# Kernel optimization log

Hardware: AMD Instinct MI355X
Metric: run time of the kernel (lower is better)

## Reference

```python
import jax, jax.numpy as jnp
import numpy as np

N_HEAD = 16
P_MIN, P_MAX = 1e-4, 1e3
V_MIN = 1e-10
SHIFT = 5.0


def setup_inputs() -> dict:
    key = jax.random.key(0)
    ks = jax.random.split(key, 4)
    B, T, C = 2, 2048, 1024
    x = jax.random.normal(ks[0], (B, T, C), dtype=jnp.float32)
    w_attn = jax.random.normal(ks[1], (C, 3 * C), dtype=jnp.float32) * 0.02
    b_attn = jnp.zeros((3 * C,), dtype=jnp.float32)
    w_proj = jax.random.normal(ks[2], (C, C), dtype=jnp.float32) * 0.02
    b_proj = jnp.zeros((C,), dtype=jnp.float32)
    p_param = jnp.ones((C,), dtype=jnp.float32)
    return {"x": x, "w_attn": w_attn, "b_attn": b_attn,
            "w_proj": w_proj, "b_proj": b_proj, "p_param": p_param}


def reference(x, w_attn, b_attn, w_proj, b_proj, p_param):
    B, T, C = x.shape
    H = N_HEAD
    d = C // H

    qkv = x @ w_attn + b_attn                      # [B,T,3C]
    q, k, v = jnp.split(qkv, 3, axis=2)

    # signed, clamped power exponent per channel: (sign(p)+0.5).sign() * clamp(|p|)
    p = jnp.sign(jnp.sign(p_param) + 0.5) * jnp.clip(jnp.abs(p_param), P_MIN, P_MAX)

    # log-power transform of V with max-subtraction over T for stability
    v = jnp.clip(jnp.abs(v + SHIFT), V_MIN, None)  # [B,T,C]
    z = p * jnp.log(v)
    z_max = jnp.max(z, axis=1, keepdims=True)      # [B,1,C]
    v = jnp.exp(z - z_max)

    # heads: [B,H,T,d]
    q = q.reshape(B, T, H, d).transpose(0, 2, 1, 3)
    k = k.reshape(B, T, H, d).transpose(0, 2, 1, 3)
    v = v.reshape(B, T, H, d).transpose(0, 2, 1, 3)

    scale = 1.0 / jnp.sqrt(jnp.float32(d))
    scores = jnp.einsum('bhqd,bhkd->bhqk', q, k) * scale
    causal = jnp.tril(jnp.ones((T, T), dtype=bool))
    scores = jnp.where(causal, scores, -jnp.inf)
    att = jax.nn.softmax(scores, axis=-1)
    mean = jnp.einsum('bhqk,bhkd->bhqd', att, v)   # [B,H,T,d]
    mean = mean.transpose(0, 2, 1, 3).reshape(B, T, C)

    # invert the log-power transform (generalized power mean)
    y = jnp.exp((z_max + jnp.log(mean)) / p) - SHIFT
    return y @ w_proj + b_proj
```

## Files before the change

### kernel.cpp

```cpp
#include <hip/hip_runtime.h>
#include <hip/hip_bf16.h>
#include <math.h>

constexpr int B_ = 2;
constexpr int T_ = 2048;
constexpr int C_ = 1024;
constexpr int H_ = 16;
constexpr int D_ = 64;
constexpr int M_ = B_ * T_;
constexpr float SHIFT_ = 5.0f;
constexpr float P_MIN_ = 1e-4f;
constexpr float P_MAX_ = 1e3f;
constexpr float V_MIN_ = 1e-10f;
typedef __attribute__((ext_vector_type(8))) short s16x8;
typedef __attribute__((ext_vector_type(4))) short s16x4;
typedef __attribute__((ext_vector_type(8))) _Float16 h16x8;
typedef __attribute__((ext_vector_type(4))) float f32x4;
typedef unsigned short ushort_t;

__device__ __forceinline__ float clamp_p(float pp) {
    float s = (pp >= 0.f) ? 1.f : -1.f;
    return s * fminf(fmaxf(fabsf(pp), P_MIN_), P_MAX_);
}

__device__ __forceinline__ ushort_t f2h(float f) {
    _Float16 h = (_Float16)f;
    return __builtin_bit_cast(unsigned short, h);
}
__device__ __forceinline__ float h2f(ushort_t h) {
    return (float)__builtin_bit_cast(_Float16, h);
}

__device__ __forceinline__ float fast_exp2(float x) {
#if __has_builtin(__builtin_amdgcn_exp2f)
    return __builtin_amdgcn_exp2f(x);
#else
    return __expf(x * 0.6931471805599453f);
#endif
}

__device__ __forceinline__ void gload_lds16(const void* g, void* l) {
    __builtin_amdgcn_global_load_lds(
        (const __attribute__((address_space(1))) unsigned int*)g,
        (__attribute__((address_space(3))) unsigned int*)l, 16, 0, 0);
}

__global__ __launch_bounds__(256)
void conv_h(const float* __restrict__ src, ushort_t* __restrict__ hi) {
    int idx = blockIdx.x * 256 + threadIdx.x;
    float4 f = ((const float4*)src)[idx];
    ushort4 h;
    h.x = f2h(f.x); h.y = f2h(f.y); h.z = f2h(f.z); h.w = f2h(f.w);
    ((ushort4*)hi)[idx] = h;
}

__global__ __launch_bounds__(256)
void convT_h(const float* __restrict__ W, ushort_t* __restrict__ Wth,
             int N, int K) {
    __shared__ float tile[64][65];
    const int k0 = blockIdx.y * 64, n0 = blockIdx.x * 64;
    const int tr = threadIdx.x >> 4;
    const int tc4 = (threadIdx.x & 15) * 4;
#pragma unroll
    for (int i = 0; i < 4; ++i) {
        float4 f = *(const float4*)&W[(size_t)(k0 + tr + i * 16) * N + n0 + tc4];
        tile[tr + i * 16][tc4 + 0] = f.x;
        tile[tr + i * 16][tc4 + 1] = f.y;
        tile[tr + i * 16][tc4 + 2] = f.z;
        tile[tr + i * 16][tc4 + 3] = f.w;
    }
    __syncthreads();
#pragma unroll
    for (int i = 0; i < 4; ++i) {
        int n = tr + i * 16;
        ushort4 h;
        h.x = f2h(tile[tc4 + 0][n]);
        h.y = f2h(tile[tc4 + 1][n]);
        h.z = f2h(tile[tc4 + 2][n]);
        h.w = f2h(tile[tc4 + 3][n]);
        *(ushort4*)&Wth[(size_t)(n0 + n) * K + k0 + tc4] = h;
    }
}

__global__ __launch_bounds__(256)
void gemm1(const ushort_t* __restrict__ Ah, const ushort_t* __restrict__ Bh,
           const float* __restrict__ bias, float* __restrict__ Cm,
           int M, int N, int K) {
    __shared__ ushort_t Lds[2 * 2 * 128 * 32];

    const int tid = threadIdx.x;
    const int w = tid >> 6;
    const int lane = tid & 63;
    const int l16 = lane & 15;
    const int quad = lane >> 4;
    const int row0 = blockIdx.y * 128, col0 = blockIdx.x * 128;
    const int wr = w >> 1, wc = w & 1;

    const ushort_t* gb[8];
    ushort_t* lb[8];
#pragma unroll
    for (int j = 0; j < 8; ++j) {
        int q = j * 4 + w;
        int plane = q >> 4;
        int cc = q & 15;
        int sub = cc & 1;
        int r = (cc >> 1) * 16 + (lane >> 2);
        const ushort_t* src = plane ? Bh : Ah;
        int tb = plane ? col0 : row0;
        gb[j] = src + (size_t)(tb + r) * K + sub * 32 + (lane & 3) * 8;
        lb[j] = &Lds[plane * 8192 + sub * 4096 + r * 32 + (lane & 3) * 8];
    }

    f32x4 acc[4][4] = {};

    for (int k0 = 0; k0 < K; k0 += 64) {
        __syncthreads();
#pragma unroll
        for (int j = 0; j < 8; ++j)
            gload_lds16(gb[j] + k0, lb[j]);
        __syncthreads();

#pragma unroll
        for (int kk = 0; kk < 2; ++kk) {
            h16x8 af[4], bf[4];
#pragma unroll
            for (int mi = 0; mi < 4; ++mi)
                af[mi] = *(const h16x8*)&Lds[kk * 4096 + (wr * 64 + mi * 16 + l16) * 32 + quad * 8];
#pragma unroll
            for (int ni = 0; ni < 4; ++ni)
                bf[ni] = *(const h16x8*)&Lds[8192 + kk * 4096 + (wc * 64 + ni * 16 + l16) * 32 + quad * 8];
#pragma unroll
            for (int mi = 0; mi < 4; ++mi)
#pragma unroll
                for (int ni = 0; ni < 4; ++ni)
                    acc[mi][ni] = __builtin_amdgcn_mfma_f32_16x16x32_f16(af[mi], bf[ni], acc[mi][ni], 0, 0, 0);
        }
    }

#pragma unroll
    for (int mi = 0; mi < 4; ++mi) {
#pragma unroll
        for (int r = 0; r < 4; ++r) {
            int row = row0 + wr * 64 + mi * 16 + quad * 4 + r;
#pragma unroll
            for (int ni = 0; ni < 4; ++ni) {
                int col = col0 + wc * 64 + ni * 16 + l16;
                Cm[(size_t)row * N + col] = acc[mi][ni][r] + bias[col];
            }
        }
    }
}

__global__ __launch_bounds__(256)
void zmax_part(const float* __restrict__ qkv, const float* __restrict__ p_param,
               float* __restrict__ zpart) {
    const int tch = blockIdx.x & 15;
    const int ctile = (blockIdx.x >> 4) & 15;
    const int b = blockIdx.x >> 8;
    const int col = threadIdx.x & 63;
    const int r = threadIdx.x >> 6;
    const int c = ctile * 64 + col;

    const float p = clamp_p(p_param[c]);
    const float* vp = qkv + (size_t)b * T_ * 3 * C_
                    + (size_t)(tch * 128) * 3 * C_ + 2 * C_ + c;

    float lm = -INFINITY;
    for (int t = r; t < 128; t += 4) {
        float v = vp[(size_t)t * 3 * C_];
        float z = p * __logf(fmaxf(fabsf(v + SHIFT_), V_MIN_));
        lm = fmaxf(lm, z);
    }
    __shared__ float red[4][64];
    red[r][col] = lm;
    __syncthreads();
    if (threadIdx.x < 64) {
        float m = fmaxf(fmaxf(red[0][threadIdx.x], red[1][threadIdx.x]),
                        fmaxf(red[2][threadIdx.x], red[3][threadIdx.x]));
        zpart[((size_t)b * 16 + tch) * C_ + ctile * 64 + threadIdx.x] = m;
    }
}

__global__ __launch_bounds__(256)
void zmax_fin(const float* __restrict__ zpart, float* __restrict__ zmax) {
    int idx = blockIdx.x * 256 + threadIdx.x;
    int b = idx >> 10;
    int c = idx & (C_ - 1);
    float m = -INFINITY;
#pragma unroll
    for (int ch = 0; ch < 16; ++ch)
        m = fmaxf(m, zpart[((size_t)b * 16 + ch) * C_ + c]);
    zmax[idx] = m;
}

__global__ __launch_bounds__(256)
void prep_kv(const float* __restrict__ qkv, const float* __restrict__ p_param,
             const float* __restrict__ zmax,
             ushort_t* __restrict__ kbf, ushort_t* __restrict__ vtbf) {
    __shared__ ushort_t VtL[64 * 72];

    const int blk = blockIdx.x;
    const int tt = blk & 31;
    const int bh = blk >> 5;
    const int b = bh >> 4;
    const int h = bh & 15;
    const int t0 = tt * 64;

    const int tl = threadIdx.x >> 2;
    const int c0 = (threadIdx.x & 3) * 16;
    const int g0 = c0 >> 3;
    const int ptl = ((tl >> 5) & 1) * 32 + ((tl >> 2) & 3) * 8
                  + ((tl >> 4) & 1) * 4 + (tl & 3);

    const size_t rowbase = (size_t)b * T_ * 3 * C_ + (size_t)(t0 + tl) * 3 * C_ + h * D_;

    {
        const float* ksrc = qkv + rowbase + C_ + c0;
        ushort_t tk[16];
#pragma unroll
        for (int u = 0; u < 16; u += 4) {
            float4 f = *(const float4*)&ksrc[u];
            tk[u + 0] = f2h(f.x); tk[u + 1] = f2h(f.y);
            tk[u + 2] = f2h(f.z); tk[u + 3] = f2h(f.w);
        }
        size_t krow = ((size_t)bh * T_ + t0 + tl) * 64;
        *(s16x8*)&kbf[krow + ((g0)     ^ (tl & 7)) * 8] = *(s16x8*)&tk[0];
        *(s16x8*)&kbf[krow + ((g0 + 1) ^ (tl & 7)) * 8] = *(s16x8*)&tk[8];
    }

    {
        const float* vsrc = qkv + rowbase + 2 * C_ + c0;
#pragma unroll
        for (int u = 0; u < 16; u += 4) {
            float4 f = *(const float4*)&vsrc[u];
            float vv[4] = {f.x, f.y, f.z, f.w};
#pragma unroll
            for (int q = 0; q < 4; ++q) {
                int c = h * D_ + c0 + u + q;
                float p = clamp_p(p_param[c]);
                float z = p * __logf(fmaxf(fabsf(vv[q] + SHIFT_), V_MIN_));
                float val = __expf(z - zmax[b * C_ + c]);
                VtL[(c0 + u + q) * 72 + ptl] = f2h(val);
            }
        }
    }
    __syncthreads();
    {
        const int d = tl;
        s16x8 r0 = *(const s16x8*)&VtL[d * 72 + c0];
        s16x8 r1 = *(const s16x8*)&VtL[d * 72 + c0 + 8];
        size_t vbase = ((size_t)bh * 32 + tt) * 4096 + (size_t)d * 64;
        *(s16x8*)&vtbf[vbase + ((g0)     ^ (d & 7)) * 8] = r0;
        *(s16x8*)&vtbf[vbase + ((g0 + 1) ^ (d & 7)) * 8] = r1;
    }
}

__device__ __forceinline__ void load_kfrag(h16x8 kf[2][4], const ushort_t* tile,
                                           int l16, int sg0, int sg1) {
#pragma unroll
    for (int nt = 0; nt < 4; ++nt) {
        kf[0][nt] = *(const h16x8*)&tile[(nt * 16 + l16) * 64 + sg0];
        kf[1][nt] = *(const h16x8*)&tile[(nt * 16 + l16) * 64 + sg1];
    }
}

__device__ __forceinline__ void tile_body2(const h16x8 qf[2][2], const h16x8 kf[2][4],
        const h16x8 vf[2][4], const h16x8 ones, bool diag, int l16, int quad, int qh,
        f32x4 O[2][4], f32x4 Ol[2]) {
#pragma unroll
    for (int m = 0; m < 2; ++m) {
        f32x4 s[4] = {};
#pragma unroll
        for (int nt = 0; nt < 4; ++nt) {
            s[nt] = __builtin_amdgcn_mfma_f32_16x16x32_f16(kf[0][nt], qf[m][0], s[nt], 0, 0, 0);
            s[nt] = __builtin_amdgcn_mfma_f32_16x16x32_f16(kf[1][nt], qf[m][1], s[nt], 0, 0, 0);
        }

        if (diag) {
            int row = qh * 32 + m * 16 + l16;
#pragma unroll
            for (int nt = 0; nt < 4; ++nt)
#pragma unroll
                for (int r = 0; r < 4; ++r) {
                    int col = nt * 16 + quad * 4 + r;
                    if (col > row) s[nt][r] = -3.0e38f;
                }
        }

#pragma unroll
        for (int ks = 0; ks < 2; ++ks) {
            ushort_t t8[8];
#pragma unroll
            for (int r = 0; r < 4; ++r) {
                t8[r]     = f2h(fast_exp2(s[2 * ks][r]));
                t8[4 + r] = f2h(fast_exp2(s[2 * ks + 1][r]));
            }
            h16x8 pa = *(const h16x8*)t8;
            Ol[m] = __builtin_amdgcn_mfma_f32_16x16x32_f16(pa, ones, Ol[m], 0, 0, 0);
#pragma unroll
            for (int nt = 0; nt < 4; ++nt)
                O[m][nt] = __builtin_amdgcn_mfma_f32_16x16x32_f16(pa, vf[ks][nt], O[m][nt], 0, 0, 0);
        }
    }
}

__global__ __launch_bounds__(256, 2)
void attn_mfma(float* qkv,
               const ushort_t* __restrict__ kbf, const ushort_t* __restrict__ vtbf,
               float* __restrict__ ml) {
    __shared__ float Osum[2][32][65];
    __shared__ float Lsum[2][32];

    const int tid = threadIdx.x;
    const int w = tid >> 6;
    const int lane = tid & 63;
    const int l16 = lane & 15;
    const int quad = lane >> 4;
    const int qh = w >> 1;
    const int kp = w & 1;

    const int qt = 31 - (blockIdx.x >> 5);
    const int bh = blockIdx.x & 31;
    const int b = bh >> 4;
    const int h = bh & 15;
    const int q0 = qt * 64;

    const int sg0 = ((0 + quad) ^ (l16 & 7)) * 8;
    const int sg1 = ((4 + quad) ^ (l16 & 7)) * 8;

    f32x4 O[2][4] = {};
    f32x4 Ol[2] = {};

    h16x8 ones;
#pragma unroll
    for (int i = 0; i < 8; ++i) ones[i] = (_Float16)1.0f;

    h16x8 qf[2][2];
#pragma unroll
    for (int m = 0; m < 2; ++m) {
        const int qrow = q0 + qh * 32 + m * 16 + l16;
        const float* qrp = qkv + (size_t)b * T_ * 3 * C_
                         + (size_t)qrow * 3 * C_ + h * D_;
#pragma unroll
        for (int ks = 0; ks < 2; ++ks) {
            const float QS = 0.125f * 1.4426950408889634f;
            float4 f0 = *(const float4*)&qrp[ks * 32 + quad * 8];
            float4 f1 = *(const float4*)&qrp[ks * 32 + quad * 8 + 4];
            ushort_t t8[8];
            t8[0] = f2h(f0.x * QS); t8[1] = f2h(f0.y * QS);
            t8[2] = f2h(f0.z * QS); t8[3] = f2h(f0.w * QS);
            t8[4] = f2h(f1.x * QS); t8[5] = f2h(f1.y * QS);
            t8[6] = f2h(f1.z * QS); t8[7] = f2h(f1.w * QS);
            qf[m][ks] = *(h16x8*)t8;
        }
    }

    const ushort_t* khead = kbf + (size_t)bh * T_ * 64;
    const ushort_t* vhead = vtbf + (size_t)bh * 32 * 4096;

    if (kp <= qt) {
        h16x8 kfA[2][4], kfB[2][4], vfA[2][4], vfB[2][4];
        load_kfrag(kfA, khead + (size_t)kp * 4096, l16, sg0, sg1);
        load_kfrag(vfA, vhead + (size_t)kp * 4096, l16, sg0, sg1);

        for (int kt = kp; kt <= qt; kt += 4) {
            int ktB = (kt + 2 <= qt) ? kt + 2 : kt;
            load_kfrag(kfB, khead + (size_t)ktB * 4096, l16, sg0, sg1);
            load_kfrag(vfB, vhead + (size_t)ktB * 4096, l16, sg0, sg1);
            tile_body2(qf, kfA, vfA, ones, kt == qt, l16, quad, qh, O, Ol);
            if (kt + 2 > qt) break;
            int ktA = (kt + 4 <= qt) ? kt + 4 : kt + 2;
            load_kfrag(kfA, khead + (size_t)ktA * 4096, l16, sg0, sg1);
            load_kfrag(vfA, vhead + (size_t)ktA * 4096, l16, sg0, sg1);
            tile_body2(qf, kfB, vfB, ones, kt + 2 == qt, l16, quad, qh, O, Ol);
        }
    }

    if (kp == 0) {
#pragma unroll
        for (int m = 0; m < 2; ++m)
#pragma unroll
            for (int r = 0; r < 4; ++r) {
                int lr = m * 16 + quad * 4 + r;
#pragma unroll
                for (int nt = 0; nt < 4; ++nt)
                    Osum[qh][lr][nt * 16 + l16] = O[m][nt][r];
                if (l16 == 0) Lsum[qh][lr] = Ol[m][r];
            }
    }
    __syncthreads();
    if (kp == 1) {
#pragma unroll
        for (int m = 0; m < 2; ++m)
#pragma unroll
            for (int r = 0; r < 4; ++r) {
                int lr = m * 16 + quad * 4 + r;
                int t = q0 + qh * 32 + lr;
                float* dst = qkv + (size_t)(b * T_ + t) * 3 * C_ + C_ + h * D_;
#pragma unroll
                for (int nt = 0; nt < 4; ++nt)
                    dst[nt * 16 + l16] = O[m][nt][r] + Osum[qh][lr][nt * 16 + l16];
                if (l16 == 0)
                    ml[bh * T_ + t] = Ol[m][r] + Lsum[qh][lr];
            }
    }
}

__global__ __launch_bounds__(256)
void combine_y(const float* __restrict__ qkv, const float* __restrict__ p_param,
               const float* __restrict__ zmax, const float* __restrict__ ml,
               ushort_t* __restrict__ yh) {
    int idx = blockIdx.x * 256 + threadIdx.x;
    int n4 = idx * 4;
    int c = n4 & (C_ - 1);
    int bt = n4 >> 10;
    int t = bt & (T_ - 1);
    int b = bt >> 11;
    int h = c >> 6;
    int bh = b * H_ + h;

    float inv_den = 1.f / ml[bh * T_ + t];

    const float* base = qkv + (size_t)bt * 3 * C_;
    float4 O0 = *(const float4*)&base[C_ + c];
    float4 zm = *(const float4*)&zmax[b * C_ + c];
    float4 pp = *(const float4*)&p_param[c];

    ushort4 hh;
    {
        float mean = O0.x * inv_den;
        float y = __expf((zm.x + __logf(mean)) / clamp_p(pp.x)) - SHIFT_;
        hh.x = f2h(y);
    }
    {
        float mean = O0.y * inv_den;
        float y = __expf((zm.y + __logf(mean)) / clamp_p(pp.y)) - SHIFT_;
        hh.y = f2h(y);
    }
    {
        float mean = O0.z * inv_den;
        float y = __expf((zm.z + __logf(mean)) / clamp_p(pp.z)) - SHIFT_;
        hh.z = f2h(y);
    }
    {
        float mean = O0.w * inv_den;
        float y = __expf((zm.w + __logf(mean)) / clamp_p(pp.w)) - SHIFT_;
        hh.w = f2h(y);
    }
    ((ushort4*)yh)[idx] = hh;
}

extern "C" void kernel_launch(void* const* d_in, const int* in_sizes, int n_in,
                              void* d_out, int out_size, void* d_ws, size_t ws_size,
                              hipStream_t stream) {
    const float* x      = (const float*)d_in[0];
    const float* w_attn = (const float*)d_in[1];
    const float* b_attn = (const float*)d_in[2];
    const float* w_proj = (const float*)d_in[3];
    const float* b_proj = (const float*)d_in[4];
    const float* p_par  = (const float*)d_in[5];
    float* out = (float*)d_out;

    char* ws = (char*)d_ws;
    float* qkv = (float*)ws;
    char* p1 = ws + (size_t)M_ * 3 * C_ * sizeof(float);
    ushort_t* xh = (ushort_t*)p1;
    ushort_t* xl = xh + (size_t)M_ * C_;
    ushort_t* wth = xl + (size_t)M_ * C_;
    ushort_t* wtl = wth + (size_t)3 * C_ * C_;
    float* zmax = (float*)(wtl + (size_t)3 * C_ * C_);
    ushort_t* kbf  = (ushort_t*)((char*)zmax + B_ * C_ * sizeof(float));
    ushort_t* vtbf = kbf + (size_t)B_ * H_ * T_ * 64;
    float* ml = (float*)(vtbf + (size_t)B_ * H_ * T_ * 64);
    float* zpart = ml + 2 * 32 * T_;

    conv_h<<<M_ * C_ / 1024, 256, 0, stream>>>(x, xh);
    convT_h<<<dim3(3 * C_ / 64, C_ / 64), 256, 0, stream>>>(w_attn, wth, 3 * C_, C_);
    gemm1<<<dim3(3 * C_ / 128, M_ / 128), 256, 0, stream>>>(xh, wth,
                                                            b_attn, qkv, M_, 3 * C_, C_);
    zmax_part<<<B_ * 16 * 16, 256, 0, stream>>>(qkv, p_par, zpart);
    zmax_fin<<<B_ * C_ / 256, 256, 0, stream>>>(zpart, zmax);
    prep_kv<<<B_ * H_ * 32, 256, 0, stream>>>(qkv, p_par, zmax, kbf, vtbf);
    attn_mfma<<<B_ * H_ * (T_ / 64), 256, 0, stream>>>(qkv, kbf, vtbf, ml);
    combine_y<<<M_ * C_ / 1024, 256, 0, stream>>>(qkv, p_par, zmax, ml, xh);
    convT_h<<<dim3(C_ / 64, C_ / 64), 256, 0, stream>>>(w_proj, wth, C_, C_);
    gemm1<<<dim3(C_ / 128, M_ / 128), 256, 0, stream>>>(xh, wth,
                                                        b_proj, out, M_, C_, C_);
}
```

Baseline: 215.7 us.

## Emit fp16 QKV from first GEMM with fused Q scaling, drop separate K repack

The QKV projection now writes fp16 instead of fp32, and the softmax scale is folded into the Q columns in its epilogue. Downstream kernels read the half-precision buffer directly: attention loads Q and K fragments straight from it, and the K-conversion pass in prep is removed. Attention output goes to a separate fp32 buffer. This halves QKV write/read traffic and removes a kernel's worth of K conversion, but K fragment loads are now strided by the 3C row pitch rather than a swizzled contiguous tile, which may hurt load efficiency. Because V is rounded to fp16 before the log, precision may also suffer.

```diff
diff --git a/kernel.cpp b/kernel.cpp
--- a/kernel.cpp
+++ b/kernel.cpp
@@ -12,8 +12,9 @@
 constexpr float P_MIN_ = 1e-4f;
 constexpr float P_MAX_ = 1e3f;
 constexpr float V_MIN_ = 1e-10f;
+constexpr float QS_ = 0.125f * 1.4426950408889634f;
+
 typedef __attribute__((ext_vector_type(8))) short s16x8;
-typedef __attribute__((ext_vector_type(4))) short s16x4;
 typedef __attribute__((ext_vector_type(8))) _Float16 h16x8;
 typedef __attribute__((ext_vector_type(4))) float f32x4;
 typedef unsigned short ushort_t;
@@ -82,10 +83,11 @@
     }
 }
 
+template <bool HALF_OUT>
 __global__ __launch_bounds__(256)
 void gemm1(const ushort_t* __restrict__ Ah, const ushort_t* __restrict__ Bh,
-           const float* __restrict__ bias, float* __restrict__ Cm,
-           int M, int N, int K) {
+           const float* __restrict__ bias, void* __restrict__ Cout,
+           int M, int N, int K, int qcols, float qscale) {
     __shared__ ushort_t Lds[2 * 2 * 128 * 32];
 
     const int tid = threadIdx.x;
@@ -137,6 +139,8 @@
         }
     }
 
+    const float osc = (HALF_OUT && col0 < qcols) ? qscale : 1.0f;
+
 #pragma unroll
     for (int mi = 0; mi < 4; ++mi) {
 #pragma unroll
@@ -145,14 +149,18 @@
 #pragma unroll
             for (int ni = 0; ni < 4; ++ni) {
                 int col = col0 + wc * 64 + ni * 16 + l16;
-                Cm[(size_t)row * N + col] = acc[mi][ni][r] + bias[col];
+                float v = acc[mi][ni][r] + bias[col];
+                if (HALF_OUT)
+                    ((ushort_t*)Cout)[(size_t)row * N + col] = f2h(v * osc);
+                else
+                    ((float*)Cout)[(size_t)row * N + col] = v;
             }
         }
     }
 }
 
 __global__ __launch_bounds__(256)
-void zmax_part(const float* __restrict__ qkv, const float* __restrict__ p_param,
+void zmax_part(const ushort_t* __restrict__ qkvh, const float* __restrict__ p_param,
                float* __restrict__ zpart) {
     const int tch = blockIdx.x & 15;
     const int ctile = (blockIdx.x >> 4) & 15;
@@ -162,12 +170,12 @@
     const int c = ctile * 64 + col;
 
     const float p = clamp_p(p_param[c]);
-    const float* vp = qkv + (size_t)b * T_ * 3 * C_
-                    + (size_t)(tch * 128) * 3 * C_ + 2 * C_ + c;
+    const ushort_t* vp = qkvh + (size_t)b * T_ * 3 * C_
+                       + (size_t)(tch * 128) * 3 * C_ + 2 * C_ + c;
 
     float lm = -INFINITY;
     for (int t = r; t < 128; t += 4) {
-        float v = vp[(size_t)t * 3 * C_];
+        float v = h2f(vp[(size_t)t * 3 * C_]);
         float z = p * __logf(fmaxf(fabsf(v + SHIFT_), V_MIN_));
         lm = fmaxf(lm, z);
     }
@@ -194,9 +202,8 @@
 }
 
 __global__ __launch_bounds__(256)
-void prep_kv(const float* __restrict__ qkv, const float* __restrict__ p_param,
-             const float* __restrict__ zmax,
-             ushort_t* __restrict__ kbf, ushort_t* __restrict__ vtbf) {
+void prep_v(const ushort_t* __restrict__ qkvh, const float* __restrict__ p_param,
+            const float* __restrict__ zmax, ushort_t* __restrict__ vtbf) {
     __shared__ ushort_t VtL[64 * 72];
 
     const int blk = blockIdx.x;
@@ -212,36 +219,20 @@
     const int ptl = ((tl >> 5) & 1) * 32 + ((tl >> 2) & 3) * 8
                   + ((tl >> 4) & 1) * 4 + (tl & 3);
 
-    const size_t rowbase = (size_t)b * T_ * 3 * C_ + (size_t)(t0 + tl) * 3 * C_ + h * D_;
-
-    {
-        const float* ksrc = qkv + rowbase + C_ + c0;
-        ushort_t tk[16];
-#pragma unroll
-        for (int u = 0; u < 16; u += 4) {
-            float4 f = *(const float4*)&ksrc[u];
-            tk[u + 0] = f2h(f.x); tk[u + 1] = f2h(f.y);
-            tk[u + 2] = f2h(f.z); tk[u + 3] = f2h(f.w);
-        }
-        size_t krow = ((size_t)bh * T_ + t0 + tl) * 64;
-        *(s16x8*)&kbf[krow + ((g0)     ^ (tl & 7)) * 8] = *(s16x8*)&tk[0];
-        *(s16x8*)&kbf[krow + ((g0 + 1) ^ (tl & 7)) * 8] = *(s16x8*)&tk[8];
-    }
-
-    {
-        const float* vsrc = qkv + rowbase + 2 * C_ + c0;
-#pragma unroll
-        for (int u = 0; u < 16; u += 4) {
-            float4 f = *(const float4*)&vsrc[u];
-            float vv[4] = {f.x, f.y, f.z, f.w};
-#pragma unroll
-            for (int q = 0; q < 4; ++q) {
-                int c = h * D_ + c0 + u + q;
-                float p = clamp_p(p_param[c]);
-                float z = p * __logf(fmaxf(fabsf(vv[q] + SHIFT_), V_MIN_));
-                float val = __expf(z - zmax[b * C_ + c]);
-                VtL[(c0 + u + q) * 72 + ptl] = f2h(val);
-            }
+    {
+        const ushort_t* vsrc = qkvh + (size_t)(b * T_ + t0 + tl) * 3 * C_
+                             + 2 * C_ + h * D_ + c0;
+        ushort_t tv[16];
+        *(s16x8*)&tv[0] = *(const s16x8*)&vsrc[0];
+        *(s16x8*)&tv[8] = *(const s16x8*)&vsrc[8];
+#pragma unroll
+        for (int q = 0; q < 16; ++q) {
+            int c = h * D_ + c0 + q;
+            float p = clamp_p(p_param[c]);
+            float v = h2f(tv[q]);
+            float z = p * __logf(fmaxf(fabsf(v + SHIFT_), V_MIN_));
+            float val = __expf(z - zmax[b * C_ + c]);
+            VtL[(c0 + q) * 72 + ptl] = f2h(val);
         }
     }
     __syncthreads();
@@ -255,12 +246,22 @@
     }
 }
 
-__device__ __forceinline__ void load_kfrag(h16x8 kf[2][4], const ushort_t* tile,
+__device__ __forceinline__ void load_kfrag(h16x8 kf[2][4], const ushort_t* krows,
+                                           int l16, int quad) {
+#pragma unroll
+    for (int nt = 0; nt < 4; ++nt) {
+        const ushort_t* rp = krows + (size_t)(nt * 16 + l16) * (3 * C_) + quad * 8;
+        kf[0][nt] = *(const h16x8*)&rp[0];
+        kf[1][nt] = *(const h16x8*)&rp[32];
+    }
+}
+
+__device__ __forceinline__ void load_vfrag(h16x8 vf[2][4], const ushort_t* tile,
                                            int l16, int sg0, int sg1) {
 #pragma unroll
     for (int nt = 0; nt < 4; ++nt) {
-        kf[0][nt] = *(const h16x8*)&tile[(nt * 16 + l16) * 64 + sg0];
-        kf[1][nt] = *(const h16x8*)&tile[(nt * 16 + l16) * 64 + sg1];
+        vf[0][nt] = *(const h16x8*)&tile[(nt * 16 + l16) * 64 + sg0];
+        vf[1][nt] = *(const h16x8*)&tile[(nt * 16 + l16) * 64 + sg1];
     }
 }
 
@@ -305,9 +306,8 @@
 }
 
 __global__ __launch_bounds__(256, 2)
-void attn_mfma(float* qkv,
-               const ushort_t* __restrict__ kbf, const ushort_t* __restrict__ vtbf,
-               float* __restrict__ ml) {
+void attn_mfma(const ushort_t* __restrict__ qkvh, const ushort_t* __restrict__ vtbf,
+               float* __restrict__ obuf, float* __restrict__ ml) {
     __shared__ float Osum[2][32][65];
     __shared__ float Lsum[2][32];
 
@@ -339,39 +339,29 @@
 #pragma unroll
     for (int m = 0; m < 2; ++m) {
         const int qrow = q0 + qh * 32 + m * 16 + l16;
-        const float* qrp = qkv + (size_t)b * T_ * 3 * C_
-                         + (size_t)qrow * 3 * C_ + h * D_;
-#pragma unroll
-        for (int ks = 0; ks < 2; ++ks) {
-            const float QS = 0.125f * 1.4426950408889634f;
-            float4 f0 = *(const float4*)&qrp[ks * 32 + quad * 8];
-            float4 f1 = *(const float4*)&qrp[ks * 32 + quad * 8 + 4];
-            ushort_t t8[8];
-            t8[0] = f2h(f0.x * QS); t8[1] = f2h(f0.y * QS);
-            t8[2] = f2h(f0.z * QS); t8[3] = f2h(f0.w * QS);
-            t8[4] = f2h(f1.x * QS); t8[5] = f2h(f1.y * QS);
-            t8[6] = f2h(f1.z * QS); t8[7] = f2h(f1.w * QS);
-            qf[m][ks] = *(h16x8*)t8;
-        }
-    }
-
-    const ushort_t* khead = kbf + (size_t)bh * T_ * 64;
+        const ushort_t* qrp = qkvh + (size_t)(b * T_ + qrow) * 3 * C_ + h * D_;
+#pragma unroll
+        for (int ks = 0; ks < 2; ++ks)
+            qf[m][ks] = *(const h16x8*)&qrp[ks * 32 + quad * 8];
+    }
+
+    const ushort_t* khead = qkvh + (size_t)b * T_ * 3 * C_ + C_ + h * D_;
     const ushort_t* vhead = vtbf + (size_t)bh * 32 * 4096;
 
     if (kp <= qt) {
         h16x8 kfA[2][4], kfB[2][4], vfA[2][4], vfB[2][4];
-        load_kfrag(kfA, khead + (size_t)kp * 4096, l16, sg0, sg1);
-        load_kfrag(vfA, vhead + (size_t)kp * 4096, l16, sg0, sg1);
+        load_kfrag(kfA, khead + (size_t)kp * 64 * 3 * C_, l16, quad);
+        load_vfrag(vfA, vhead + (size_t)kp * 4096, l16, sg0, sg1);
 
         for (int kt = kp; kt <= qt; kt += 4) {
             int ktB = (kt + 2 <= qt) ? kt + 2 : kt;
-            load_kfrag(kfB, khead + (size_t)ktB * 4096, l16, sg0, sg1);
-            load_kfrag(vfB, vhead + (size_t)ktB * 4096, l16, sg0, sg1);
+            load_kfrag(kfB, khead + (size_t)ktB * 64 * 3 * C_, l16, quad);
+            load_vfrag(vfB, vhead + (size_t)ktB * 4096, l16, sg0, sg1);
             tile_body2(qf, kfA, vfA, ones, kt == qt, l16, quad, qh, O, Ol);
             if (kt + 2 > qt) break;
             int ktA = (kt + 4 <= qt) ? kt + 4 : kt + 2;
-            load_kfrag(kfA, khead + (size_t)ktA * 4096, l16, sg0, sg1);
-            load_kfrag(vfA, vhead + (size_t)ktA * 4096, l16, sg0, sg1);
+            load_kfrag(kfA, khead + (size_t)ktA * 64 * 3 * C_, l16, quad);
+            load_vfrag(vfA, vhead + (size_t)ktA * 4096, l16, sg0, sg1);
             tile_body2(qf, kfB, vfB, ones, kt + 2 == qt, l16, quad, qh, O, Ol);
         }
     }
@@ -396,7 +386,7 @@
             for (int r = 0; r < 4; ++r) {
                 int lr = m * 16 + quad * 4 + r;
                 int t = q0 + qh * 32 + lr;
-                float* dst = qkv + (size_t)(b * T_ + t) * 3 * C_ + C_ + h * D_;
+                float* dst = obuf + (size_t)(b * T_ + t) * C_ + h * D_;
 #pragma unroll
                 for (int nt = 0; nt < 4; ++nt)
                     dst[nt * 16 + l16] = O[m][nt][r] + Osum[qh][lr][nt * 16 + l16];
@@ -407,7 +397,7 @@
 }
 
 __global__ __launch_bounds__(256)
-void combine_y(const float* __restrict__ qkv, const float* __restrict__ p_param,
+void combine_y(const float* __restrict__ obuf, const float* __restrict__ p_param,
                const float* __restrict__ zmax, const float* __restrict__ ml,
                ushort_t* __restrict__ yh) {
     int idx = blockIdx.x * 256 + threadIdx.x;
@@ -421,8 +411,7 @@
 
     float inv_den = 1.f / ml[bh * T_ + t];
 
-    const float* base = qkv + (size_t)bt * 3 * C_;
-    float4 O0 = *(const float4*)&base[C_ + c];
+    float4 O0 = *(const float4*)&obuf[(size_t)bt * C_ + c];
     float4 zm = *(const float4*)&zmax[b * C_ + c];
     float4 pp = *(const float4*)&p_param[c];
 
@@ -462,28 +451,25 @@
     float* out = (float*)d_out;
 
     char* ws = (char*)d_ws;
-    float* qkv = (float*)ws;
-    char* p1 = ws + (size_t)M_ * 3 * C_ * sizeof(float);
-    ushort_t* xh = (ushort_t*)p1;
-    ushort_t* xl = xh + (size_t)M_ * C_;
-    ushort_t* wth = xl + (size_t)M_ * C_;
-    ushort_t* wtl = wth + (size_t)3 * C_ * C_;
-    float* zmax = (float*)(wtl + (size_t)3 * C_ * C_);
-    ushort_t* kbf  = (ushort_t*)((char*)zmax + B_ * C_ * sizeof(float));
-    ushort_t* vtbf = kbf + (size_t)B_ * H_ * T_ * 64;
+    ushort_t* qkvh = (ushort_t*)ws;
+    ushort_t* xh   = qkvh + (size_t)M_ * 3 * C_;
+    ushort_t* wth  = xh + (size_t)M_ * C_;
+    float* obuf = (float*)(wth + (size_t)3 * C_ * C_);
+    float* zmax = obuf + (size_t)M_ * C_;
+    ushort_t* vtbf = (ushort_t*)(zmax + B_ * C_);
     float* ml = (float*)(vtbf + (size_t)B_ * H_ * T_ * 64);
-    float* zpart = ml + 2 * 32 * T_;
+    float* zpart = ml + 32 * T_;
 
     conv_h<<<M_ * C_ / 1024, 256, 0, stream>>>(x, xh);
     convT_h<<<dim3(3 * C_ / 64, C_ / 64), 256, 0, stream>>>(w_attn, wth, 3 * C_, C_);
-    gemm1<<<dim3(3 * C_ / 128, M_ / 128), 256, 0, stream>>>(xh, wth,
-                                                            b_attn, qkv, M_, 3 * C_, C_);
-    zmax_part<<<B_ * 16 * 16, 256, 0, stream>>>(qkv, p_par, zpart);
+    gemm1<true><<<dim3(3 * C_ / 128, M_ / 128), 256, 0, stream>>>(
+        xh, wth, b_attn, qkvh, M_, 3 * C_, C_, C_, QS_);
+    zmax_part<<<B_ * 16 * 16, 256, 0, stream>>>(qkvh, p_par, zpart);
     zmax_fin<<<B_ * C_ / 256, 256, 0, stream>>>(zpart, zmax);
-    prep_kv<<<B_ * H_ * 32, 256, 0, stream>>>(qkv, p_par, zmax, kbf, vtbf);
-    attn_mfma<<<B_ * H_ * (T_ / 64), 256, 0, stream>>>(qkv, kbf, vtbf, ml);
-    combine_y<<<M_ * C_ / 1024, 256, 0, stream>>>(qkv, p_par, zmax, ml, xh);
+    prep_v<<<B_ * H_ * 32, 256, 0, stream>>>(qkvh, p_par, zmax, vtbf);
+    attn_mfma<<<B_ * H_ * (T_ / 64), 256, 0, stream>>>(qkvh, vtbf, obuf, ml);
+    combine_y<<<M_ * C_ / 1024, 256, 0, stream>>>(obuf, p_par, zmax, ml, xh);
     convT_h<<<dim3(C_ / 64, C_ / 64), 256, 0, stream>>>(w_proj, wth, C_, C_);
-    gemm1<<<dim3(C_ / 128, M_ / 128), 256, 0, stream>>>(xh, wth,
-                                                        b_proj, out, M_, C_, C_);
-}
+    gemm1<false><<<dim3(C_ / 128, M_ / 128), 256, 0, stream>>>(
+        xh, wth, b_proj, out, M_, C_, C_, 0, 1.0f);
+}
```

Result: slower. 241.4 us (+11.9%).
